# Performance work log

Hardware: AMD Instinct MI355X
Metric: run time of the kernel (lower is better)

The kernel has to match this reference:

```python
import jax, jax.numpy as jnp
import numpy as np

B, S, E, H, MAXLEN = 2, 2048, 1024, 16, 2048


def _level_indices(seq_len: int, base: int = 2) -> np.ndarray:
    """Vectorized version of get_level_index_weak over the full (target, source) grid.
    indices[t, s] = min(level, 2) for s < t, else 0. Runs in O(log S) passes."""
    tt = np.broadcast_to(np.arange(seq_len)[:, None], (seq_len, seq_len)).astype(np.int64).copy()
    ss = np.broadcast_to(np.arange(seq_len)[None, :], (seq_len, seq_len)).astype(np.int64).copy()
    res = np.zeros((seq_len, seq_len), np.int64)
    done = ~(ss < tt)  # only source < target positions get a level; rest stay 0
    while not done.all():
        l = np.floor(np.log2(np.maximum(tt, 1).astype(np.float64))).astype(np.int64)
        v = (np.int64(1) << l)
        hit = (~done) & (ss < v)
        res[hit] = l[hit] + 1
        done |= hit
        step = ~done
        tt[step] -= v[step]
        ss[step] -= v[step]
    return np.minimum(res, 2).astype(np.int32)


def setup_inputs() -> dict:
    key = jax.random.key(0)
    ks = jax.random.split(key, 10)
    sc = 0.02
    return {
        "x": jax.random.normal(ks[0], (B, S, E), dtype=jnp.float32),
        "attention_mask": jax.random.randint(ks[1], (B, S), 0, 2, dtype=jnp.int32),
        "level_indices": jnp.asarray(_level_indices(S, 2)),
        "Wq": jax.random.normal(ks[2], (E, E), dtype=jnp.float32) * sc,
        "bq": jnp.zeros((E,), jnp.float32),
        "Wk": jax.random.normal(ks[3], (E, E), dtype=jnp.float32) * sc,
        "bk": jnp.zeros((E,), jnp.float32),
        "Wv": jax.random.normal(ks[4], (E, E), dtype=jnp.float32) * sc,
        "bv": jnp.zeros((E,), jnp.float32),
        "hier": jax.random.normal(ks[5], (MAXLEN, H, 3), dtype=jnp.float32),
        "Wo": jax.random.normal(ks[6], (E, E), dtype=jnp.float32) * sc,
        "bo": jnp.zeros((E,), jnp.float32),
    }


def reference(x, attention_mask, level_indices, Wq, bq, Wk, bk, Wv, bv, hier, Wo, bo):
    b, s, e = x.shape
    h = hier.shape[1]
    dh = e // h
    # q/k are computed by the original module but never used; kept for fidelity (zero grads).
    q = x @ Wq.T + bq
    k = x @ Wk.T + bk
    v = (x @ Wv.T + bv).reshape(b, s, h, dh).transpose(0, 2, 1, 3)  # [B,H,S,Dh]
    lev = level_indices[:s, :s]  # [S,S] int, values in {0,1,2}
    # Faithful torch.gather semantics: weights[b,h,i,j] = hier[b, h, lev[i,j]]
    w3 = hier[:b]                      # [B,H,3]
    weights = w3[:, :, lev]            # [B,H,S,S]
    decay = jnp.power(jnp.float32(0.5), lev.astype(x.dtype))  # [S,S]
    weights = weights * decay
    weights = weights / (jnp.sum(weights, axis=-1, keepdims=True) + 1e-8)
    weights = jnp.where(attention_mask[:, None, None, :] == 0, jnp.float32(0.0), weights)
    out = jnp.einsum('bhij,bhjd->bhid', weights, v)  # [B,H,S,Dh]
    out = out.transpose(0, 2, 1, 3).reshape(b, s, e)
    return out @ Wo.T + bo
```

## Files before the change

### kernel.cpp

```cpp
#include <hip/hip_runtime.h>
#include <cstdint>
#include <cstddef>

constexpr int Sn = 2048;
constexpr int En = 1024;
constexpr int Bn = 2;
constexpr int Hn = 16;
constexpr int NCH = 32;
constexpr int CHUNK = 64;
constexpr int Mtot = Bn * Sn;
constexpr int GCH = Mtot / CHUNK;

typedef __bf16 bf16x8 __attribute__((ext_vector_type(8)));
typedef float  f32x4  __attribute__((ext_vector_type(4)));

__device__ __forceinline__ unsigned short f2bf(float f) {
    union { float f; uint32_t u; } v; v.f = f;
    const uint32_t u = v.u;
    return (unsigned short)((u + 0x7fffu + ((u >> 16) & 1u)) >> 16);
}
__device__ __forceinline__ float bf2f(unsigned short s) {
    union { uint32_t u; float f; } v; v.u = (uint32_t)s << 16; return v.f;
}

constexpr int XN = Bn * Sn * En;
constexpr int WN = En * En;

__global__ __launch_bounds__(256)
void cast3(const float* __restrict__ x, const float* __restrict__ Wv,
           const float* __restrict__ Wo, unsigned short* __restrict__ xb,
           unsigned short* __restrict__ Wvb, unsigned short* __restrict__ Wob)
{
    const int i = (blockIdx.x * 256 + threadIdx.x) * 4;
    const float* src; unsigned short* dst; int off;
    if (i < XN)           { src = x;  dst = xb;  off = i; }
    else if (i < XN + WN) { src = Wv; dst = Wvb; off = i - XN; }
    else                  { src = Wo; dst = Wob; off = i - XN - WN; }
    const float4 v = *(const float4*)(src + off);
    ushort4 o;
    o.x = f2bf(v.x); o.y = f2bf(v.y); o.z = f2bf(v.z); o.w = f2bf(v.w);
    *(ushort4*)(dst + off) = o;
}

#define LOAD6(k0, r0, r1, r2, r3, r4, r5)            \
    r0 = *(const uint4*)(gA0 + (k0));                \
    r1 = *(const uint4*)(gA0 + (k0) + 32);           \
    r2 = *(const uint4*)(gA1 + (k0));                \
    r3 = *(const uint4*)(gA1 + (k0) + 32);           \
    r4 = *(const uint4*)(gB0 + (k0));                \
    r5 = *(const uint4*)(gB0 + (k0) + 32);

#define STORE6(r0, r1, r2, r3, r4, r5)               \
    *lA00 = r0; *lA01 = r1;                          \
    *lA10 = r2; *lA11 = r3;                          \
    *lB00 = r4; *lB01 = r5;

#define COMPUTE()                                                                              \
    {                                                                                          \
        bf16x8 af[4][2], bfr[2][2];                                                            \
        _Pragma("unroll")                                                                      \
        for (int i = 0; i < 4; ++i)                                                            \
            _Pragma("unroll")                                                                  \
            for (int kh = 0; kh < 2; ++kh)                                                     \
                af[i][kh] = *(const bf16x8*)&As[((wr * 4 + i) * 2 + kh) * 512 + lane * 8];      \
        _Pragma("unroll")                                                                      \
        for (int j = 0; j < 2; ++j)                                                            \
            _Pragma("unroll")                                                                  \
            for (int kh = 0; kh < 2; ++kh)                                                     \
                bfr[j][kh] = *(const bf16x8*)&Bs[((wc * 2 + j) * 2 + kh) * 512 + lane * 8];     \
        _Pragma("unroll")                                                                      \
        for (int kh = 0; kh < 2; ++kh)                                                         \
            _Pragma("unroll")                                                                  \
            for (int i = 0; i < 4; ++i)                                                        \
                _Pragma("unroll")                                                              \
                for (int j = 0; j < 2; ++j)                                                    \
                    acc[i][j] = __builtin_amdgcn_mfma_f32_16x16x32_bf16(af[i][kh], bfr[j][kh], \
                                                                        acc[i][j], 0, 0, 0);   \
    }

template<bool APPLY_MASK, bool OUT_BF16, bool FUSE_CSUM>
__global__ __launch_bounds__(256)
void gemm_pipe(const unsigned short* __restrict__ A, const unsigned short* __restrict__ Bw,
               const float* __restrict__ bias, const int* __restrict__ mask,
               void* __restrict__ Cv, float* __restrict__ csum, int M, int N, int K)
{
    __shared__ __align__(16) unsigned short As[128 * 64];
    __shared__ __align__(16) unsigned short Bs[64 * 64];

    const int tid  = threadIdx.x;
    const int lane = tid & 63;
    const int wv   = tid >> 6;
    const int wr   = wv >> 1;
    const int wc   = wv & 1;
    const int id   = blockIdx.y * 16 + blockIdx.x;
    const int xcd  = id & 7;
    const int slot = id >> 3;
    const int by   = xcd * 4 + (slot >> 4);
    const int bx   = slot & 15;
    const int bm   = by * 128;
    const int bn   = bx * 64;
    const int m16  = lane & 15;
    const int kq   = lane >> 4;

    f32x4 acc[4][2] = {};

    const int rg0 = 2 * wv, rg1 = 2 * wv + 1;
    const unsigned short* gA0 = A  + (size_t)(bm + 16 * rg0 + m16) * K + kq * 8;
    const unsigned short* gA1 = A  + (size_t)(bm + 16 * rg1 + m16) * K + kq * 8;
    const unsigned short* gB0 = Bw + (size_t)(bn + 16 * wv  + m16) * K + kq * 8;
    uint4* lA00 = (uint4*)&As[(rg0 * 2 + 0) * 512 + lane * 8];
    uint4* lA01 = (uint4*)&As[(rg0 * 2 + 1) * 512 + lane * 8];
    uint4* lA10 = (uint4*)&As[(rg1 * 2 + 0) * 512 + lane * 8];
    uint4* lA11 = (uint4*)&As[(rg1 * 2 + 1) * 512 + lane * 8];
    uint4* lB00 = (uint4*)&Bs[(wv  * 2 + 0) * 512 + lane * 8];
    uint4* lB01 = (uint4*)&Bs[(wv  * 2 + 1) * 512 + lane * 8];

    uint4 p0, p1, p2, p3, p4, p5;
    uint4 q0, q1, q2, q3, q4, q5;

    LOAD6(0, p0, p1, p2, p3, p4, p5);
#pragma unroll 1
    for (int it = 0; it < 8; ++it) {
        const int kbase = it * 128;
        __syncthreads();
        STORE6(p0, p1, p2, p3, p4, p5);
        __syncthreads();
        LOAD6(kbase + 64, q0, q1, q2, q3, q4, q5);
        COMPUTE();

        __syncthreads();
        STORE6(q0, q1, q2, q3, q4, q5);
        __syncthreads();
        if (it < 7) { LOAD6(kbase + 128, p0, p1, p2, p3, p4, p5); }
        COMPUTE();
    }

    float colsum[2] = {0.0f, 0.0f};
#pragma unroll
    for (int i = 0; i < 4; ++i) {
        const int r0 = bm + wr * 64 + i * 16 + kq * 4;
#pragma unroll
        for (int j = 0; j < 2; ++j) {
            const int c0 = bn + wc * 32 + j * 16 + m16;
            const float bcol = bias[c0];
#pragma unroll
            for (int r = 0; r < 4; ++r) {
                const int row = r0 + r;
                float val = acc[i][j][r] + bcol;
                if (APPLY_MASK) val = (mask[row] == 0) ? 0.0f : val;
                if (FUSE_CSUM) colsum[j] += val;
                if (OUT_BF16)
                    ((unsigned short*)Cv)[(size_t)row * N + c0] = f2bf(val);
                else
                    ((float*)Cv)[(size_t)row * N + c0] = val;
            }
        }
    }

    if (FUSE_CSUM) {
        const int gc = 2 * by + wr;
#pragma unroll
        for (int j = 0; j < 2; ++j) {
            float s = colsum[j];
            s += __shfl_xor(s, 16, 64);
            s += __shfl_xor(s, 32, 64);
            if (kq == 0)
                csum[(size_t)gc * En + bn + wc * 32 + j * 16 + m16] = s;
        }
    }
}

__global__ __launch_bounds__(256)
void combine(const unsigned short* __restrict__ vm, const float* __restrict__ csum,
             const float* __restrict__ hier, unsigned short* __restrict__ opre)
{
    const int e = blockIdx.x * 256 + threadIdx.x;
    const int c = blockIdx.y;
    const int b = blockIdx.z;
    const int h = e >> 6;

    const float w0 = hier[((size_t)b * Hn + h) * 3 + 0];
    const float w1 = hier[((size_t)b * Hn + h) * 3 + 1] * 0.5f;
    const float w2 = hier[((size_t)b * Hn + h) * 3 + 2] * 0.25f;

    float run = 0.0f, T = 0.0f;
    const int g0 = b * NCH;
    for (int c2 = 0; c2 < NCH; ++c2) {
        const float v = csum[(size_t)(g0 + c2) * En + e];
        if (c2 < c) run += v;
        T += v;
    }

    float prev = 0.0f;
    const size_t base = ((size_t)b * Sn + c * CHUNK) * En + e;

    for (int t = 0; t < CHUNK; ++t) {
        const int i = c * CHUNK + t;
        const float cur = bf2f(vm[base + (size_t)t * En]);
        float num, Z;
        if (i & 1) {
            num = w2 * (run - prev) + w1 * prev + w0 * (T - run);
            Z = (float)(i - 1) * w2 + w1 + (float)(Sn - i) * w0 + 1e-8f;
        } else {
            num = w2 * run + w0 * (T - run);
            Z = (float)i * w2 + (float)(Sn - i) * w0 + 1e-8f;
        }
        opre[base + (size_t)t * En] = f2bf(num / Z);
        run += cur;
        prev = cur;
    }
}

extern "C" void kernel_launch(void* const* d_in, const int* in_sizes, int n_in,
                              void* d_out, int out_size, void* d_ws, size_t ws_size,
                              hipStream_t stream)
{
    const float* x    = (const float*)d_in[0];
    const int*   mask = (const int*)d_in[1];
    const float* Wv   = (const float*)d_in[7];
    const float* bv   = (const float*)d_in[8];
    const float* hier = (const float*)d_in[9];
    const float* Wo   = (const float*)d_in[10];
    const float* bo   = (const float*)d_in[11];
    float* out = (float*)d_out;

    const int M = Mtot, N = En, K = En;

    char* ws = (char*)d_ws;
    unsigned short* xb    = (unsigned short*)ws;  ws += (size_t)M * K * 2;
    unsigned short* Wvb   = (unsigned short*)ws;  ws += (size_t)N * K * 2;
    unsigned short* Wob   = (unsigned short*)ws;  ws += (size_t)N * K * 2;
    unsigned short* vmb   = (unsigned short*)ws;  ws += (size_t)M * N * 2;
    float*          csum  = (float*)ws;           ws += (size_t)GCH * En * 4;
    unsigned short* opreb = (unsigned short*)ws;  ws += (size_t)M * N * 2;

    dim3 threads(256);

    cast3<<<dim3((XN + 2 * WN) / 1024), threads, 0, stream>>>(x, Wv, Wo, xb, Wvb, Wob);

    dim3 gemm_grid(16, 32);

    gemm_pipe<true, true, true><<<gemm_grid, threads, 0, stream>>>(xb, Wvb, bv, mask, vmb, csum, M, N, K);
    combine<<<dim3(En / 256, NCH, Bn), threads, 0, stream>>>(vmb, csum, hier, opreb);
    gemm_pipe<false, false, false><<<gemm_grid, threads, 0, stream>>>(opreb, Wob, bo, nullptr, out, nullptr, M, N, K);
}
```

Before: 169.1 us.

## Switch GEMMs to 64x64 tiles with direct global-to-LDS loads

```diff
diff --git a/kernel.cpp b/kernel.cpp
--- a/kernel.cpp
+++ b/kernel.cpp
@@ -6,13 +6,16 @@
 constexpr int En = 1024;
 constexpr int Bn = 2;
 constexpr int Hn = 16;
-constexpr int NCH = 32;
-constexpr int CHUNK = 64;
+constexpr int CHUNK = 32;
+constexpr int NCH = Sn / CHUNK;
 constexpr int Mtot = Bn * Sn;
 constexpr int GCH = Mtot / CHUNK;
 
 typedef __bf16 bf16x8 __attribute__((ext_vector_type(8)));
 typedef float  f32x4  __attribute__((ext_vector_type(4)));
+
+#define GLOBAL_AS(p) ((const __attribute__((address_space(1))) void*)(p))
+#define LDS_AS(p)    ((__attribute__((address_space(3))) void*)(p))
 
 __device__ __forceinline__ unsigned short f2bf(float f) {
     union { float f; uint32_t u; } v; v.f = f;
@@ -42,49 +45,13 @@
     *(ushort4*)(dst + off) = o;
 }
 
-#define LOAD6(k0, r0, r1, r2, r3, r4, r5)            \
-    r0 = *(const uint4*)(gA0 + (k0));                \
-    r1 = *(const uint4*)(gA0 + (k0) + 32);           \
-    r2 = *(const uint4*)(gA1 + (k0));                \
-    r3 = *(const uint4*)(gA1 + (k0) + 32);           \
-    r4 = *(const uint4*)(gB0 + (k0));                \
-    r5 = *(const uint4*)(gB0 + (k0) + 32);
-
-#define STORE6(r0, r1, r2, r3, r4, r5)               \
-    *lA00 = r0; *lA01 = r1;                          \
-    *lA10 = r2; *lA11 = r3;                          \
-    *lB00 = r4; *lB01 = r5;
-
-#define COMPUTE()                                                                              \
-    {                                                                                          \
-        bf16x8 af[4][2], bfr[2][2];                                                            \
-        _Pragma("unroll")                                                                      \
-        for (int i = 0; i < 4; ++i)                                                            \
-            _Pragma("unroll")                                                                  \
-            for (int kh = 0; kh < 2; ++kh)                                                     \
-                af[i][kh] = *(const bf16x8*)&As[((wr * 4 + i) * 2 + kh) * 512 + lane * 8];      \
-        _Pragma("unroll")                                                                      \
-        for (int j = 0; j < 2; ++j)                                                            \
-            _Pragma("unroll")                                                                  \
-            for (int kh = 0; kh < 2; ++kh)                                                     \
-                bfr[j][kh] = *(const bf16x8*)&Bs[((wc * 2 + j) * 2 + kh) * 512 + lane * 8];     \
-        _Pragma("unroll")                                                                      \
-        for (int kh = 0; kh < 2; ++kh)                                                         \
-            _Pragma("unroll")                                                                  \
-            for (int i = 0; i < 4; ++i)                                                        \
-                _Pragma("unroll")                                                              \
-                for (int j = 0; j < 2; ++j)                                                    \
-                    acc[i][j] = __builtin_amdgcn_mfma_f32_16x16x32_bf16(af[i][kh], bfr[j][kh], \
-                                                                        acc[i][j], 0, 0, 0);   \
-    }
-
 template<bool APPLY_MASK, bool OUT_BF16, bool FUSE_CSUM>
-__global__ __launch_bounds__(256)
-void gemm_pipe(const unsigned short* __restrict__ A, const unsigned short* __restrict__ Bw,
-               const float* __restrict__ bias, const int* __restrict__ mask,
-               void* __restrict__ Cv, float* __restrict__ csum, int M, int N, int K)
-{
-    __shared__ __align__(16) unsigned short As[128 * 64];
+__global__ __launch_bounds__(256, 4)
+void gemm64(const unsigned short* __restrict__ A, const unsigned short* __restrict__ Bw,
+            const float* __restrict__ bias, const int* __restrict__ mask,
+            void* __restrict__ Cv, float* __restrict__ csum, int M, int N, int K)
+{
+    __shared__ __align__(16) unsigned short As[64 * 64];
     __shared__ __align__(16) unsigned short Bs[64 * 64];
 
     const int tid  = threadIdx.x;
@@ -95,50 +62,52 @@
     const int id   = blockIdx.y * 16 + blockIdx.x;
     const int xcd  = id & 7;
     const int slot = id >> 3;
-    const int by   = xcd * 4 + (slot >> 4);
+    const int by   = xcd * 8 + (slot >> 4);
     const int bx   = slot & 15;
-    const int bm   = by * 128;
+    const int bm   = by * 64;
     const int bn   = bx * 64;
     const int m16  = lane & 15;
     const int kq   = lane >> 4;
 
-    f32x4 acc[4][2] = {};
-
-    const int rg0 = 2 * wv, rg1 = 2 * wv + 1;
-    const unsigned short* gA0 = A  + (size_t)(bm + 16 * rg0 + m16) * K + kq * 8;
-    const unsigned short* gA1 = A  + (size_t)(bm + 16 * rg1 + m16) * K + kq * 8;
-    const unsigned short* gB0 = Bw + (size_t)(bn + 16 * wv  + m16) * K + kq * 8;
-    uint4* lA00 = (uint4*)&As[(rg0 * 2 + 0) * 512 + lane * 8];
-    uint4* lA01 = (uint4*)&As[(rg0 * 2 + 1) * 512 + lane * 8];
-    uint4* lA10 = (uint4*)&As[(rg1 * 2 + 0) * 512 + lane * 8];
-    uint4* lA11 = (uint4*)&As[(rg1 * 2 + 1) * 512 + lane * 8];
-    uint4* lB00 = (uint4*)&Bs[(wv  * 2 + 0) * 512 + lane * 8];
-    uint4* lB01 = (uint4*)&Bs[(wv  * 2 + 1) * 512 + lane * 8];
-
-    uint4 p0, p1, p2, p3, p4, p5;
-    uint4 q0, q1, q2, q3, q4, q5;
-
-    LOAD6(0, p0, p1, p2, p3, p4, p5);
+    f32x4 acc[2][2] = {};
+
+    const unsigned short* gA = A  + (size_t)(bm + 16 * wv + m16) * K + kq * 8;
+    const unsigned short* gB = Bw + (size_t)(bn + 16 * wv + m16) * K + kq * 8;
+    unsigned short* lA0 = &As[(wv * 2 + 0) * 512];
+    unsigned short* lA1 = &As[(wv * 2 + 1) * 512];
+    unsigned short* lB0 = &Bs[(wv * 2 + 0) * 512];
+    unsigned short* lB1 = &Bs[(wv * 2 + 1) * 512];
+
 #pragma unroll 1
-    for (int it = 0; it < 8; ++it) {
-        const int kbase = it * 128;
+    for (int k0 = 0; k0 < K; k0 += 64) {
         __syncthreads();
-        STORE6(p0, p1, p2, p3, p4, p5);
+        __builtin_amdgcn_global_load_lds(GLOBAL_AS(gA + k0),      LDS_AS(lA0), 16, 0, 0);
+        __builtin_amdgcn_global_load_lds(GLOBAL_AS(gA + k0 + 32), LDS_AS(lA1), 16, 0, 0);
+        __builtin_amdgcn_global_load_lds(GLOBAL_AS(gB + k0),      LDS_AS(lB0), 16, 0, 0);
+        __builtin_amdgcn_global_load_lds(GLOBAL_AS(gB + k0 + 32), LDS_AS(lB1), 16, 0, 0);
         __syncthreads();
-        LOAD6(kbase + 64, q0, q1, q2, q3, q4, q5);
-        COMPUTE();
-
-        __syncthreads();
-        STORE6(q0, q1, q2, q3, q4, q5);
-        __syncthreads();
-        if (it < 7) { LOAD6(kbase + 128, p0, p1, p2, p3, p4, p5); }
-        COMPUTE();
+
+        bf16x8 af[2][2], bfr[2][2];
+#pragma unroll
+        for (int i = 0; i < 2; ++i)
+#pragma unroll
+            for (int kh = 0; kh < 2; ++kh) {
+                af[i][kh]  = *(const bf16x8*)&As[((2 * wr + i) * 2 + kh) * 512 + lane * 8];
+                bfr[i][kh] = *(const bf16x8*)&Bs[((2 * wc + i) * 2 + kh) * 512 + lane * 8];
+            }
+#pragma unroll
+        for (int kh = 0; kh < 2; ++kh)
+#pragma unroll
+            for (int i = 0; i < 2; ++i)
+#pragma unroll
+                for (int j = 0; j < 2; ++j)
+                    acc[i][j] = __builtin_amdgcn_mfma_f32_16x16x32_bf16(af[i][kh], bfr[j][kh], acc[i][j], 0, 0, 0);
     }
 
     float colsum[2] = {0.0f, 0.0f};
 #pragma unroll
-    for (int i = 0; i < 4; ++i) {
-        const int r0 = bm + wr * 64 + i * 16 + kq * 4;
+    for (int i = 0; i < 2; ++i) {
+        const int r0 = bm + wr * 32 + i * 16 + kq * 4;
 #pragma unroll
         for (int j = 0; j < 2; ++j) {
             const int c0 = bn + wc * 32 + j * 16 + m16;
@@ -238,9 +207,9 @@
 
     cast3<<<dim3((XN + 2 * WN) / 1024), threads, 0, stream>>>(x, Wv, Wo, xb, Wvb, Wob);
 
-    dim3 gemm_grid(16, 32);
-
-    gemm_pipe<true, true, true><<<gemm_grid, threads, 0, stream>>>(xb, Wvb, bv, mask, vmb, csum, M, N, K);
+    dim3 gemm_grid(16, 64);
+
+    gemm64<true, true, true><<<gemm_grid, threads, 0, stream>>>(xb, Wvb, bv, mask, vmb, csum, M, N, K);
     combine<<<dim3(En / 256, NCH, Bn), threads, 0, stream>>>(vmb, csum, hier, opreb);
-    gemm_pipe<false, false, false><<<gemm_grid, threads, 0, stream>>>(opreb, Wob, bo, nullptr, out, nullptr, M, N, K);
-}
+    gemm64<false, false, false><<<gemm_grid, threads, 0, stream>>>(opreb, Wob, bo, nullptr, out, nullptr, M, N, K);
+}
```

Result: slower. 181.4 us (+7.3%).
